# Kernel tuning notes

Hardware: AMD Instinct MI355X
Metric: run time of the kernel (lower is better)

## Reference

```python
import jax, jax.numpy as jnp
import numpy as np

D = 1024      # neural_dim
M = 8192      # memory_size (assumed fully used)
H = 16        # num_heads
B = 64        # batch
HD = D // H   # head dim


def setup_inputs() -> dict:
    key = jax.random.key(0)
    ks = jax.random.split(key, 24)
    s = 0.02
    inp = {
        "neural_input": jax.random.normal(ks[0], (B, D), jnp.float32),
        "memory_keys": jax.random.normal(ks[1], (M, D), jnp.float32),
        "memory_values": jax.random.normal(ks[2], (M, D), jnp.float32),
        # query/key/value projections (nn.Linear weights are [out, in])
        "Wq": jax.random.normal(ks[3], (D, D), jnp.float32) * s,
        "bq": jnp.zeros((D,), jnp.float32),
        "Wk": jax.random.normal(ks[4], (D, D), jnp.float32) * s,
        "bk": jnp.zeros((D,), jnp.float32),
        "Wv": jax.random.normal(ks[5], (D, D), jnp.float32) * s,
        "bv": jnp.zeros((D,), jnp.float32),
        # MultiheadAttention packed in-projection [3D, D] and out projection
        "in_proj_w": jax.random.normal(ks[6], (3 * D, D), jnp.float32) * s,
        "in_proj_b": jnp.zeros((3 * D,), jnp.float32),
        "out_w": jax.random.normal(ks[7], (D, D), jnp.float32) * s,
        "out_b": jnp.zeros((D,), jnp.float32),
        # memory_gate: Linear(2D->D), ReLU, Linear(D->D), Sigmoid
        "gW1": jax.random.normal(ks[8], (D, 2 * D), jnp.float32) * s,
        "gb1": jnp.zeros((D,), jnp.float32),
        "gW2": jax.random.normal(ks[9], (D, D), jnp.float32) * s,
        "gb2": jnp.zeros((D,), jnp.float32),
        # integration: Linear(2D->2D), ReLU, Linear(2D->D)
        "iW1": jax.random.normal(ks[10], (2 * D, 2 * D), jnp.float32) * s,
        "ib1": jnp.zeros((2 * D,), jnp.float32),
        "iW2": jax.random.normal(ks[11], (D, 2 * D), jnp.float32) * s,
        "ib2": jnp.zeros((D,), jnp.float32),
    }
    return inp


def reference(neural_input, memory_keys, memory_values,
              Wq, bq, Wk, bk, Wv, bv,
              in_proj_w, in_proj_b, out_w, out_b,
              gW1, gb1, gW2, gb2, iW1, ib1, iW2, ib2):
    x = neural_input  # [B, D]
    # pre-projections (memory_used assumed all True -> full tables)
    q = x @ Wq.T + bq                  # [B, D]
    k = memory_keys @ Wk.T + bk        # [M, D]
    v = memory_values @ Wv.T + bv      # [M, D]

    # MultiheadAttention (single query per batch element; K/V shared
    # across batch instead of the redundant expand in the original)
    Wiq, Wik, Wiv = in_proj_w[:D], in_proj_w[D:2 * D], in_proj_w[2 * D:]
    biq, bik, biv = in_proj_b[:D], in_proj_b[D:2 * D], in_proj_b[2 * D:]
    qh = (q @ Wiq.T + biq).reshape(B, H, HD)   # [B, H, hd]
    kh = (k @ Wik.T + bik).reshape(M, H, HD)   # [M, H, hd]
    vh = (v @ Wiv.T + biv).reshape(M, H, HD)   # [M, H, hd]

    scale = 1.0 / np.sqrt(HD).astype(np.float32)
    scores = jnp.einsum('bhd,mhd->bhm', qh, kh) * scale  # [B, H, M]
    attn = jax.nn.softmax(scores, axis=-1)
    ctx = jnp.einsum('bhm,mhd->bhd', attn, vh).reshape(B, D)
    memory_signal = ctx @ out_w.T + out_b      # [B, D]

    # gated fusion
    gate_in = jnp.concatenate([x, memory_signal], axis=-1)          # [B, 2D]
    gate = jax.nn.sigmoid(jax.nn.relu(gate_in @ gW1.T + gb1) @ gW2.T + gb2)
    gated_memory = gate * memory_signal
    combined = jnp.concatenate([x, gated_memory], axis=-1)          # [B, 2D]
    out = jax.nn.relu(combined @ iW1.T + ib1) @ iW2.T + ib2         # [B, D]
    return out
```

## Files before the change

kernel.cpp:

```cpp
#include <hip/hip_runtime.h>
#include <hip/hip_bf16.h>
#include <stdint.h>


typedef __bf16 bf16;
typedef __bf16 bf16x4 __attribute__((ext_vector_type(4)));
typedef __bf16 bf16x8 __attribute__((ext_vector_type(8)));
typedef float f32x4 __attribute__((ext_vector_type(4)));

#define D_ 1024
#define M_ 8192
#define B_ 64
#define H_ 16

static __device__ __forceinline__ void gload16(const void* g, void* l) {
  __builtin_amdgcn_global_load_lds(
      (const __attribute__((address_space(1))) void*)g,
      (__attribute__((address_space(3))) void*)l, 16, 0, 0);
}

static __device__ __forceinline__ f32x4 mfma16(bf16x8 a, bf16x8 b, f32x4 c) {
  return __builtin_amdgcn_mfma_f32_16x16x32_bf16(a, b, c, 0, 0, 0);
}

template <int U, int KLEN, typename OutT>
__device__ __forceinline__ void thin_gemm(
    const bf16* __restrict__ A, int lda,
    const bf16* __restrict__ Bm, int ldb,
    OutT* __restrict__ C, int ldc,
    const float* __restrict__ bias, float scale) {
  const int tid = threadIdx.x, lane = tid & 63, w = tid >> 6;
  const int rl = lane & 15, qq = lane >> 4;
  const bf16* pa = A + (int64_t)(w * 16 + rl) * lda + qq * 8;
  const bf16* pb[4];
  pb[0] = Bm + (int64_t)rl * ldb + qq * 8;
  pb[1] = pb[0] + (int64_t)16 * ldb;
  pb[2] = pb[0] + (int64_t)32 * ldb;
  pb[3] = pb[0] + (int64_t)48 * ldb;
  f32x4 acc[4] = {};
  bf16x8 av[2][U], bv[2][U][4];
#pragma unroll
  for (int u = 0; u < U; u++) {
    av[0][u] = *(const bf16x8*)(pa + u * 32);
#pragma unroll
    for (int j = 0; j < 4; j++)
      bv[0][u][j] = *(const bf16x8*)(pb[j] + u * 32);
  }
  constexpr int NI = KLEN / (32 * U);
#pragma unroll
  for (int it = 0; it < NI; it++) {
    const int cur = it & 1, nxt = cur ^ 1;
    if (it + 1 < NI) {
      int k = (it + 1) * 32 * U;
#pragma unroll
      for (int u = 0; u < U; u++) {
        av[nxt][u] = *(const bf16x8*)(pa + k + u * 32);
#pragma unroll
        for (int j = 0; j < 4; j++)
          bv[nxt][u][j] = *(const bf16x8*)(pb[j] + k + u * 32);
      }
    }
#pragma unroll
    for (int u = 0; u < U; u++)
#pragma unroll
      for (int j = 0; j < 4; j++)
        acc[j] = mfma16(av[cur][u], bv[cur][u][j], acc[j]);
  }
#pragma unroll
  for (int j = 0; j < 4; j++) {
    int gn = j * 16 + rl;
    float bb = bias ? bias[gn] : 0.0f;
#pragma unroll
    for (int r = 0; r < 4; r++) {
      int gm = w * 16 + qq * 4 + r;
      C[(int64_t)gm * ldc + gn] = (OutT)((acc[j][r] + bb) * scale);
    }
  }
}

struct CvtD { const float* src; bf16* dst; int end; };
struct PrepArgs {
  CvtD d[9];
  const float *Wq, *Wk, *Wv, *inw, *inb, *bq, *bk, *bv;
  const float *outb, *gb1, *gb2, *ib1, *ib2;
  bf16* WT;
  float *bc, *msR, *g1R, *gateR, *h1R, *out, *Oraw, *lmat;
};

__global__ __launch_bounds__(256) void prep_kernel(PrepArgs a) {
  const int bx = blockIdx.x, tid = threadIdx.x;
  if (bx < 29760) {
    int g = bx * 256 + tid;
    CvtD dd = a.d[8];
    int begin = a.d[7].end;
#pragma unroll
    for (int t = 7; t >= 0; t--)
      if (g < a.d[t].end) { dd = a.d[t]; begin = t ? a.d[t - 1].end : 0; }
    int i = (g - begin) * 4;
    float4 v = *(const float4*)(dd.src + i);
    bf16x4 o = { (bf16)v.x, (bf16)v.y, (bf16)v.z, (bf16)v.w };
    *(bf16x4*)(dd.dst + i) = o;
  } else if (bx < 32832) {
    int t = bx - 29760;
    int z = t >> 10, rem = t & 1023;
    const float* src = z == 0 ? a.Wq : z == 1 ? a.Wk : a.Wv;
    bf16* out = a.WT + (int64_t)z * D_ * D_;
    __shared__ bf16 tile[32][33];
    int tx = tid & 31, ty = tid >> 5;
    int r0 = (rem >> 5) * 32, c0 = (rem & 31) * 32;
#pragma unroll
    for (int i = 0; i < 32; i += 8)
      tile[ty + i][tx] = (bf16)src[(int64_t)(r0 + ty + i) * D_ + c0 + tx];
    __syncthreads();
#pragma unroll
    for (int i = 0; i < 32; i += 8)
      out[(int64_t)(c0 + ty + i) * D_ + r0 + tx] = tile[tx][ty + i];
  } else if (bx < 33600) {
    int t = bx - 32832;
    int w = tid >> 6, lane = tid & 63;
    int ng = t * 4 + w;
    int z = ng >> 10;
    const float* Wi = a.inw + (int64_t)ng * D_;
    const float* b = z == 0 ? a.bq : z == 1 ? a.bk : a.bv;
    float acc = 0.f;
#pragma unroll
    for (int l = 0; l < D_; l += 64) acc += Wi[l + lane] * b[l + lane];
#pragma unroll
    for (int m = 32; m; m >>= 1) acc += __shfl_xor(acc, m, 64);
    if (lane == 0) a.bc[ng] = acc + a.inb[ng];
  } else if (bx < 33984) {
    int t = bx - 33600;
    int seg = t >> 6, row = t & 63;
    int n = tid * 4;
    const float* b;
    float* dst;
    int bn = n;
    if (seg == 0)      { dst = a.msR   + row * 1024;        b = a.outb; }
    else if (seg == 1) { dst = a.g1R   + row * 1024;        b = a.gb1;  }
    else if (seg == 2) { dst = a.gateR + row * 1024;        b = a.gb2;  }
    else if (seg == 3) { dst = a.h1R   + row * 2048;        b = a.ib1;  }
    else if (seg == 4) { dst = a.h1R   + row * 2048 + 1024; b = a.ib1; bn = 1024 + n; }
    else               { dst = a.out   + row * 1024;        b = a.ib2;  }
    *(float4*)(dst + n) = *(const float4*)(b + bn);
  } else {
    int b = bx - 33984;
    float4 z4 = {0.f, 0.f, 0.f, 0.f};
    *(float4*)(a.Oraw + b * 1024 + tid * 4) = z4;
    if (b < 16 && tid < 64) a.lmat[b * 64 + tid] = 0.f;
  }
}

template <int MODE>
__global__ __launch_bounds__(256) void gemm_big(
    const bf16* __restrict__ A, int lda, int64_t sA,
    const bf16* __restrict__ Bm, int ldb, int64_t sB,
    bf16* __restrict__ C, int ldc, int64_t sC, bf16* __restrict__ Ct,
    const float* __restrict__ bias, int64_t sbias, int K,
    const bf16* __restrict__ qA, const bf16* __restrict__ qB,
    bf16* __restrict__ qC, const float* __restrict__ qbias) {
  int m0, n0, z;
  if (MODE == 0) {
    z = blockIdx.z; m0 = blockIdx.y * 128; n0 = blockIdx.x * 128;
  } else {
    if ((int)blockIdx.x >= 1024) {
      int n0q = ((int)blockIdx.x - 1024) * 64;
      thin_gemm<2, 1024, bf16>(qA, D_, qB + (int64_t)n0q * D_, D_,
                               qC + n0q, D_, qbias + n0q, 0.125f);
      return;
    }
    int lin = blockIdx.x, xcd = lin & 7, slot = lin >> 3;
    z = slot >> 6;
    int r = slot & 63;
    m0 = (xcd * 8 + (r >> 3)) * 128;
    n0 = (r & 7) * 128;
  }
  A += (int64_t)z * sA; Bm += (int64_t)z * sB;
  if (bias) bias += (int64_t)z * sbias;
  __shared__ alignas(16) bf16 As[128 * 32];
  __shared__ alignas(16) bf16 Bs[128 * 32];
  const int tid = threadIdx.x, lane = tid & 63, w = tid >> 6;
  const int wm = (w & 1) * 64, wn = (w >> 1) * 64;
  const int rl = lane & 15, qq = lane >> 4;
  f32x4 acc[4][4] = {};

  int c0 = w * 64 + lane, c1 = (4 + w) * 64 + lane;
  int ra0 = c0 >> 2, qa0 = (c0 & 3) ^ ((ra0 >> 1) & 3);
  int ra1 = c1 >> 2, qa1 = (c1 & 3) ^ ((ra1 >> 1) & 3);
  const bf16* gA0 = A + (int64_t)(m0 + ra0) * lda + qa0 * 8;
  const bf16* gA1 = A + (int64_t)(m0 + ra1) * lda + qa1 * 8;
  const bf16* gB0 = Bm + (int64_t)(n0 + ra0) * ldb + qa0 * 8;
  const bf16* gB1 = Bm + (int64_t)(n0 + ra1) * ldb + qa1 * 8;
  bf16* lA0 = As + w * 512;
  bf16* lA1 = As + (4 + w) * 512;
  bf16* lB0 = Bs + w * 512;
  bf16* lB1 = Bs + (4 + w) * 512;

  for (int k0 = 0; k0 < K; k0 += 32) {
    __syncthreads();
    gload16(gA0 + k0, lA0);
    gload16(gA1 + k0, lA1);
    gload16(gB0 + k0, lB0);
    gload16(gB1 + k0, lB1);
    __syncthreads();
    bf16x8 af[4], bb[4];
#pragma unroll
    for (int i = 0; i < 4; i++) {
      int r = wm + i * 16 + rl;
      af[i] = *(const bf16x8*)(As + r * 32 + (qq ^ ((r >> 1) & 3)) * 8);
    }
#pragma unroll
    for (int j = 0; j < 4; j++) {
      int r = wn + j * 16 + rl;
      bb[j] = *(const bf16x8*)(Bs + r * 32 + (qq ^ ((r >> 1) & 3)) * 8);
    }
#pragma unroll
    for (int i = 0; i < 4; i++)
#pragma unroll
      for (int j = 0; j < 4; j++)
        acc[i][j] = mfma16(af[i], bb[j], acc[i][j]);
  }
  if (MODE == 1 && z == 1) {
#pragma unroll
    for (int j = 0; j < 4; j++) {
      int gn = n0 + wn + j * 16 + rl;
      float bb2 = bias ? bias[gn] : 0.0f;
#pragma unroll
      for (int i = 0; i < 4; i++) {
        int gm0 = m0 + wm + i * 16 + qq * 4;
        f32x4 a = acc[i][j];
        bf16x4 o = { (bf16)(a[0] + bb2), (bf16)(a[1] + bb2),
                     (bf16)(a[2] + bb2), (bf16)(a[3] + bb2) };
        *(bf16x4*)(Ct + (int64_t)gn * M_ + gm0) = o;
      }
    }
  } else {
    C += (int64_t)z * sC;
#pragma unroll
    for (int j = 0; j < 4; j++) {
      int gn = n0 + wn + j * 16 + rl;
      float bb2 = bias ? bias[gn] : 0.0f;
#pragma unroll
      for (int i = 0; i < 4; i++) {
        int gm0 = m0 + wm + i * 16 + qq * 4;
#pragma unroll
        for (int r = 0; r < 4; r++)
          C[(int64_t)(gm0 + r) * ldc + gn] = (bf16)(acc[i][j][r] + bb2);
      }
    }
  }
}

__global__ __launch_bounds__(256, 2) void flash_kernel(
    const bf16* __restrict__ qh, const bf16* __restrict__ kh,
    const bf16* __restrict__ vhT, float* __restrict__ Oraw,
    float* __restrict__ lmat) {
  const int tid = threadIdx.x, lane = tid & 63, w = tid >> 6;
  const int rl = lane & 15, qq = lane >> 4;
  const int h = blockIdx.x >> 4, c = blockIdx.x & 15;
  __shared__ alignas(16) bf16 Plds[4 * 16 * 72];
  const bf16* qhp = qh + (int64_t)(w * 16 + rl) * D_ + h * 64 + qq * 8;
  bf16x8 aq0 = *(const bf16x8*)(qhp);
  bf16x8 aq1 = *(const bf16x8*)(qhp + 32);
  float lsum[4] = {0.f, 0.f, 0.f, 0.f};
  f32x4 acc_o[4] = {};
  bf16* pl = Plds + w * 1152;
  const bf16* khb = kh + (int64_t)(c * 512) * D_ + h * 64 + qq * 8;
  const bf16* vtb = vhT + (int64_t)(h * 64) * M_ + c * 512 + qq * 8;
  for (int nt = 0; nt < 8; nt++) {
    int mb = nt * 64;
    bf16x8 bk0[4], bk1[4], vv0[4], vv1[4];
#pragma unroll
    for (int j = 0; j < 4; j++) {
      const bf16* p = khb + (int64_t)(mb + j * 16 + rl) * D_;
      bk0[j] = *(const bf16x8*)(p);
      bk1[j] = *(const bf16x8*)(p + 32);
      const bf16* q = vtb + (int64_t)(j * 16 + rl) * M_ + mb;
      vv0[j] = *(const bf16x8*)(q);
      vv1[j] = *(const bf16x8*)(q + 32);
    }
    f32x4 s[4] = {};
#pragma unroll
    for (int j = 0; j < 4; j++) {
      s[j] = mfma16(aq0, bk0[j], s[j]);
      s[j] = mfma16(aq1, bk1[j], s[j]);
    }
#pragma unroll
    for (int j = 0; j < 4; j++)
#pragma unroll
      for (int r = 0; r < 4; r++) {
        float p = __expf(s[j][r]);
        lsum[r] += p;
        pl[(qq * 4 + r) * 72 + j * 16 + rl] = (bf16)p;
      }
    bf16x8 pa0 = *(const bf16x8*)(pl + rl * 72 + qq * 8);
    bf16x8 pa1 = *(const bf16x8*)(pl + rl * 72 + 32 + qq * 8);
#pragma unroll
    for (int j = 0; j < 4; j++) {
      acc_o[j] = mfma16(pa0, vv0[j], acc_o[j]);
      acc_o[j] = mfma16(pa1, vv1[j], acc_o[j]);
    }
  }
#pragma unroll
  for (int msk = 1; msk <= 8; msk <<= 1)
#pragma unroll
    for (int r = 0; r < 4; r++) lsum[r] += __shfl_xor(lsum[r], msk, 64);
#pragma unroll
  for (int j = 0; j < 4; j++)
#pragma unroll
    for (int r = 0; r < 4; r++)
      atomicAdd(&Oraw[(int64_t)(w * 16 + qq * 4 + r) * D_ + h * 64 + j * 16 + rl],
                acc_o[j][r]);
  if (rl == 0)
#pragma unroll
    for (int r = 0; r < 4; r++)
      atomicAdd(&lmat[h * 64 + w * 16 + qq * 4 + r], lsum[r]);
}

struct Chunk { const void* p0; const void* p1; int ld; int kind; };
struct StageArgs { Chunk c[16]; };

template <int NKK>
__global__ __launch_bounds__(256) void tail_stage(
    StageArgs sa, const bf16* __restrict__ Bw, int ldb,
    float* __restrict__ Craw, int ldc) {
  const int n0 = blockIdx.x * 64, kc = blockIdx.y;
  const int bk0 = kc * NKK * 32;
  const Chunk ch = sa.c[kc];
  const int tid = threadIdx.x, lane = tid & 63, w = tid >> 6;
  const int rl = lane & 15, qq = lane >> 4;
  const int m = w * 16 + rl;
  const bf16* pb[4];
#pragma unroll
  for (int j = 0; j < 4; j++)
    pb[j] = Bw + (int64_t)(n0 + j * 16 + rl) * ldb + bk0 + qq * 8;
  f32x4 acc[4] = {};
#pragma unroll
  for (int kk = 0; kk < NKK; kk++) {
    bf16x8 af;
    if (ch.kind == 0) {
      af = *(const bf16x8*)((const bf16*)ch.p0 + (int64_t)m * ch.ld +
                            kk * 32 + qq * 8);
    } else {
      const float* p = (const float*)ch.p0 + (int64_t)m * ch.ld + kk * 32 + qq * 8;
      float4 u0 = *(const float4*)p;
      float4 u1 = *(const float4*)(p + 4);
      if (ch.kind == 2) {
        u0.x = fmaxf(u0.x, 0.f); u0.y = fmaxf(u0.y, 0.f);
        u0.z = fmaxf(u0.z, 0.f); u0.w = fmaxf(u0.w, 0.f);
        u1.x = fmaxf(u1.x, 0.f); u1.y = fmaxf(u1.y, 0.f);
        u1.z = fmaxf(u1.z, 0.f); u1.w = fmaxf(u1.w, 0.f);
      } else if (ch.kind == 3) {
        const float* pm = (const float*)ch.p1 + (int64_t)m * ch.ld + kk * 32 + qq * 8;
        float4 m0 = *(const float4*)pm;
        float4 m1 = *(const float4*)(pm + 4);
        u0.x = m0.x / (1.f + __expf(-u0.x)); u0.y = m0.y / (1.f + __expf(-u0.y));
        u0.z = m0.z / (1.f + __expf(-u0.z)); u0.w = m0.w / (1.f + __expf(-u0.w));
        u1.x = m1.x / (1.f + __expf(-u1.x)); u1.y = m1.y / (1.f + __expf(-u1.y));
        u1.z = m1.z / (1.f + __expf(-u1.z)); u1.w = m1.w / (1.f + __expf(-u1.w));
      } else if (ch.kind == 4) {
        int hidx = (bk0 + kk * 32) >> 6;
        float linv = 1.0f / ((const float*)ch.p1)[hidx * 64 + m];
        u0.x *= linv; u0.y *= linv; u0.z *= linv; u0.w *= linv;
        u1.x *= linv; u1.y *= linv; u1.z *= linv; u1.w *= linv;
      }
      af = (bf16x8){ (bf16)u0.x, (bf16)u0.y, (bf16)u0.z, (bf16)u0.w,
                     (bf16)u1.x, (bf16)u1.y, (bf16)u1.z, (bf16)u1.w };
    }
    bf16x8 bf_[4];
#pragma unroll
    for (int j = 0; j < 4; j++) bf_[j] = *(const bf16x8*)(pb[j] + kk * 32);
#pragma unroll
    for (int j = 0; j < 4; j++) acc[j] = mfma16(af, bf_[j], acc[j]);
  }
#pragma unroll
  for (int j = 0; j < 4; j++) {
    int gn = n0 + j * 16 + rl;
#pragma unroll
    for (int r = 0; r < 4; r++) {
      int gm = w * 16 + qq * 4 + r;
      atomicAdd(&Craw[(int64_t)gm * ldc + gn], acc[j][r]);
    }
  }
}

extern "C" void kernel_launch(void* const* d_in, const int* in_sizes, int n_in,
                              void* d_out, int out_size, void* d_ws,
                              size_t ws_size, hipStream_t stream) {
  (void)in_sizes; (void)n_in; (void)out_size;
  const float* x    = (const float*)d_in[0];
  const float* mk   = (const float*)d_in[1];
  const float* mv   = (const float*)d_in[2];
  const float* Wq   = (const float*)d_in[3];
  const float* bq   = (const float*)d_in[4];
  const float* Wk   = (const float*)d_in[5];
  const float* bk   = (const float*)d_in[6];
  const float* Wv   = (const float*)d_in[7];
  const float* bv   = (const float*)d_in[8];
  const float* inw  = (const float*)d_in[9];
  const float* inb  = (const float*)d_in[10];
  const float* outw = (const float*)d_in[11];
  const float* outb = (const float*)d_in[12];
  const float* gW1  = (const float*)d_in[13];
  const float* gb1  = (const float*)d_in[14];
  const float* gW2  = (const float*)d_in[15];
  const float* gb2  = (const float*)d_in[16];
  const float* iW1  = (const float*)d_in[17];
  const float* ib1  = (const float*)d_in[18];
  const float* iW2  = (const float*)d_in[19];
  const float* ib2  = (const float*)d_in[20];

  char* ws = (char*)d_ws;
  size_t off = 0;
  auto alloc = [&](size_t bytes) {
    char* p = ws + off;
    off += (bytes + 255) & ~(size_t)255;
    return p;
  };
  bf16* mkmv  = (bf16*)alloc((size_t)2 * M_ * D_ * 2);
  bf16* inpj  = (bf16*)alloc((size_t)3 * D_ * D_ * 2);
  bf16* WT    = (bf16*)alloc((size_t)3 * D_ * D_ * 2);
  bf16* Wc    = (bf16*)alloc((size_t)3 * D_ * D_ * 2);
  float* bc   = (float*)alloc(3 * D_ * 4);
  bf16* xbf   = (bf16*)alloc((size_t)B_ * D_ * 2);
  bf16* qh    = (bf16*)alloc((size_t)B_ * D_ * 2);
  bf16* kh    = (bf16*)alloc((size_t)M_ * D_ * 2);
  bf16* vhT   = (bf16*)alloc((size_t)M_ * D_ * 2);
  float* Oraw = (float*)alloc((size_t)B_ * D_ * 4);
  float* lmat = (float*)alloc((size_t)H_ * B_ * 4);
  float* msR  = (float*)alloc((size_t)B_ * D_ * 4);
  float* g1R  = (float*)alloc((size_t)B_ * D_ * 4);
  float* gateR= (float*)alloc((size_t)B_ * D_ * 4);
  float* h1R  = (float*)alloc((size_t)B_ * 2 * D_ * 4);
  bf16* gW1b  = (bf16*)alloc((size_t)D_ * 2 * D_ * 2);
  bf16* gW2b  = (bf16*)alloc((size_t)D_ * D_ * 2);
  bf16* iW1b  = (bf16*)alloc((size_t)2 * D_ * 2 * D_ * 2);
  bf16* iW2b  = (bf16*)alloc((size_t)D_ * 2 * D_ * 2);
  bf16* outwb = (bf16*)alloc((size_t)D_ * D_ * 2);
  if (ws_size < off) return;

  PrepArgs pa;
  pa.d[0] = { mk,   mkmv,           2097152 };
  pa.d[1] = { mv,   mkmv + M_ * D_, 4194304 };
  pa.d[2] = { inw,  inpj,           4980736 };
  pa.d[3] = { gW1,  gW1b,           5505024 };
  pa.d[4] = { gW2,  gW2b,           5767168 };
  pa.d[5] = { iW1,  iW1b,           6815744 };
  pa.d[6] = { iW2,  iW2b,           7340032 };
  pa.d[7] = { outw, outwb,          7602176 };
  pa.d[8] = { x,    xbf,            7618560 };
  pa.Wq = Wq; pa.Wk = Wk; pa.Wv = Wv; pa.inw = inw; pa.inb = inb;
  pa.bq = bq; pa.bk = bk; pa.bv = bv;
  pa.outb = outb; pa.gb1 = gb1; pa.gb2 = gb2; pa.ib1 = ib1; pa.ib2 = ib2;
  pa.WT = WT; pa.bc = bc; pa.msR = msR; pa.g1R = g1R; pa.gateR = gateR;
  pa.h1R = h1R; pa.out = (float*)d_out; pa.Oraw = Oraw; pa.lmat = lmat;
  prep_kernel<<<dim3(34048), 256, 0, stream>>>(pa);

  gemm_big<0><<<dim3(8, 8, 3), 256, 0, stream>>>(
      inpj, D_, (int64_t)D_ * D_, WT, D_, (int64_t)D_ * D_,
      Wc, D_, (int64_t)D_ * D_, nullptr, nullptr, 0, D_,
      nullptr, nullptr, nullptr, nullptr);

  gemm_big<1><<<dim3(1040), 256, 0, stream>>>(
      mkmv, D_, (int64_t)M_ * D_, Wc + (int64_t)D_ * D_, D_, (int64_t)D_ * D_,
      kh, D_, 0, vhT, bc + D_, D_, D_,
      xbf, Wc, qh, bc);

  flash_kernel<<<dim3(256), 256, 0, stream>>>(qh, kh, vhT, Oraw, lmat);

  StageArgs s1;
  for (int kc = 0; kc < 8; kc++) s1.c[kc] = { Oraw + kc * 128, lmat, D_, 4 };
  tail_stage<4><<<dim3(16, 8), 256, 0, stream>>>(s1, outwb, D_, msR, D_);

  StageArgs s2;
  for (int kc = 0; kc < 8; kc++)  s2.c[kc] = { xbf + kc * 128, nullptr, D_, 0 };
  for (int kc = 8; kc < 16; kc++) s2.c[kc] = { msR + (kc - 8) * 128, nullptr, D_, 1 };
  tail_stage<4><<<dim3(16, 16), 256, 0, stream>>>(s2, gW1b, 2 * D_, g1R, D_);

  StageArgs s3;
  for (int kc = 0; kc < 8; kc++) s3.c[kc] = { g1R + kc * 128, nullptr, D_, 2 };
  tail_stage<4><<<dim3(16, 8), 256, 0, stream>>>(s3, gW2b, D_, gateR, D_);

  StageArgs s4;
  for (int kc = 0; kc < 8; kc++)  s4.c[kc] = { xbf + kc * 128, nullptr, D_, 0 };
  for (int kc = 8; kc < 16; kc++)
    s4.c[kc] = { gateR + (kc - 8) * 128, msR + (kc - 8) * 128, D_, 3 };
  tail_stage<4><<<dim3(32, 16), 256, 0, stream>>>(s4, iW1b, 2 * D_, h1R, 2 * D_);

  StageArgs s5;
  for (int kc = 0; kc < 16; kc++) s5.c[kc] = { h1R + kc * 128, nullptr, 2 * D_, 2 };
  tail_stage<4><<<dim3(16, 16), 256, 0, stream>>>(s5, iW2b, 2 * D_,
                                                  (float*)d_out, D_);
}
```

Baseline: 354.2 us.

## Replace big K/V projection GEMM with 256x256-tile 4-stage pipelined kernel

Adds a new gemm256 kernel that computes the memory-key and memory-value projections with 256x256 output tiles, 512 threads, and a 4-deep LDS ring buffer fed by direct global-to-LDS loads with XOR swizzle. Blocks are mapped so that tiles are grouped per XCD, and the q projection rides along in the first 16 blocks. Larger tiles raise arithmetic intensity and cut redundant operand traffic compared to the previous 1040-block launch, at the cost of 128KB dynamic LDS per block and a large register-resident accumulator, which limits occupancy to one block per CU. The v output is written transposed with 4-wide vector stores, while the k output still uses scalar stores.

```diff
diff --git a/kernel.cpp b/kernel.cpp
--- a/kernel.cpp
+++ b/kernel.cpp
@@ -248,6 +248,146 @@
       }
     }
   }
+}
+
+__global__ __launch_bounds__(512) void gemm256(
+    const bf16* __restrict__ A,
+    const bf16* __restrict__ Wc,
+    const float* __restrict__ bc,
+    bf16* __restrict__ kh, bf16* __restrict__ vhT,
+    const bf16* __restrict__ qA, const bf16* __restrict__ qB,
+    bf16* __restrict__ qC, const float* __restrict__ qbias) {
+  extern __shared__ __align__(16) bf16 lds[];
+  const int bid = blockIdx.x;
+  if (bid < 16) {
+    if (threadIdx.x < 256) {
+      int n0q = bid * 64;
+      thin_gemm<2, 1024, bf16>(qA, D_, qB + (int64_t)n0q * D_, D_,
+                               qC + n0q, D_, qbias + n0q, 0.125f);
+    }
+    return;
+  }
+  const int lin = bid - 16;
+  const int xcd = lin & 7, s = lin >> 3;
+  const int z = xcd >> 2;
+  const int m0 = ((xcd & 3) * 8 + (s >> 2)) * 256;
+  const int n0 = (s & 3) * 256;
+  const bf16* Ab = A + (int64_t)z * M_ * D_;
+  const bf16* Bb = Wc + (int64_t)(z + 1) * D_ * D_;
+  const float* bias = bc + (z + 1) * D_;
+
+  const int tid = threadIdx.x, lane = tid & 63, w = tid >> 6;
+  const int rl = lane & 15, qq = lane >> 4;
+  const int wr = w >> 2, wcn = w & 3;
+
+  const int ci0 = w * 128 + lane, ci1 = ci0 + 64;
+  const int ra0 = ci0 >> 2, ca0 = (ci0 & 3) ^ ((ra0 >> 1) & 3);
+  const int ra1 = ci1 >> 2, ca1 = (ci1 & 3) ^ ((ra1 >> 1) & 3);
+  const bf16* gA0 = Ab + (int64_t)(m0 + ra0) * D_ + ca0 * 8;
+  const bf16* gA1 = Ab + (int64_t)(m0 + ra1) * D_ + ca1 * 8;
+  const bf16* gB0 = Bb + (int64_t)(n0 + ra0) * D_ + ca0 * 8;
+  const bf16* gB1 = Bb + (int64_t)(n0 + ra1) * D_ + ca1 * 8;
+  const int lA0 = w * 1024, lA1 = lA0 + 512;
+
+#define STAGE3(kt)                                   \
+  do {                                               \
+    bf16* bse = lds + ((kt) & 3) * 16384;            \
+    int ko = (kt) * 32;                              \
+    gload16(gA0 + ko, bse + lA0);                    \
+    gload16(gA1 + ko, bse + lA1);                    \
+    gload16(gB0 + ko, bse + 8192 + lA0);             \
+    gload16(gB1 + ko, bse + 8192 + lA1);             \
+  } while (0)
+#define FENCE3 asm volatile("" ::: "memory")
+#define BARRIER3                       \
+  do {                                 \
+    FENCE3;                            \
+    __builtin_amdgcn_s_barrier();      \
+    FENCE3;                            \
+  } while (0)
+
+  f32x4 acc[8][4] = {};
+  const int sq8 = (qq ^ ((rl >> 1) & 3)) * 8;
+
+  auto compute = [&](int kt) {
+    const bf16* ba = lds + (kt & 3) * 16384;
+    const bf16* bbp = ba + 8192;
+    bf16x8 bfr[4], afr[4];
+#pragma unroll
+    for (int j = 0; j < 4; j++)
+      bfr[j] = *(const bf16x8*)(bbp + (wcn * 64 + j * 16 + rl) * 32 + sq8);
+#pragma unroll
+    for (int mi = 0; mi < 4; mi++)
+      afr[mi] = *(const bf16x8*)(ba + (wr * 128 + mi * 16 + rl) * 32 + sq8);
+    __builtin_amdgcn_s_setprio(1);
+#pragma unroll
+    for (int mi = 0; mi < 4; mi++)
+#pragma unroll
+      for (int j = 0; j < 4; j++)
+        acc[mi][j] = mfma16(afr[mi], bfr[j], acc[mi][j]);
+    __builtin_amdgcn_s_setprio(0);
+#pragma unroll
+    for (int mi = 0; mi < 4; mi++)
+      afr[mi] = *(const bf16x8*)(ba + (wr * 128 + (mi + 4) * 16 + rl) * 32 + sq8);
+    __builtin_amdgcn_s_setprio(1);
+#pragma unroll
+    for (int mi = 0; mi < 4; mi++)
+#pragma unroll
+      for (int j = 0; j < 4; j++)
+        acc[mi + 4][j] = mfma16(afr[mi], bfr[j], acc[mi + 4][j]);
+    __builtin_amdgcn_s_setprio(0);
+  };
+
+  constexpr int NT = 32;
+  STAGE3(0);
+  STAGE3(1);
+  STAGE3(2);
+#pragma unroll 1
+  for (int kt = 0; kt < NT - 2; kt++) {
+    if (kt + 3 < NT) STAGE3(kt + 3);
+    asm volatile("s_waitcnt vmcnt(8)" ::: "memory");
+    BARRIER3;
+    compute(kt);
+    BARRIER3;
+  }
+  asm volatile("s_waitcnt vmcnt(4)" ::: "memory");
+  BARRIER3;
+  compute(NT - 2);
+  asm volatile("s_waitcnt vmcnt(0)" ::: "memory");
+  BARRIER3;
+  compute(NT - 1);
+
+  if (z == 0) {
+#pragma unroll
+    for (int j = 0; j < 4; j++) {
+      int gn = n0 + wcn * 64 + j * 16 + rl;
+      float bb2 = bias[gn];
+#pragma unroll
+      for (int mi = 0; mi < 8; mi++) {
+        int gm0 = m0 + wr * 128 + mi * 16 + qq * 4;
+#pragma unroll
+        for (int r = 0; r < 4; r++)
+          kh[(int64_t)(gm0 + r) * D_ + gn] = (bf16)(acc[mi][j][r] + bb2);
+      }
+    }
+  } else {
+#pragma unroll
+    for (int j = 0; j < 4; j++) {
+      int gn = n0 + wcn * 64 + j * 16 + rl;
+      float bb2 = bias[gn];
+#pragma unroll
+      for (int mi = 0; mi < 8; mi++) {
+        int gm0 = m0 + wr * 128 + mi * 16 + qq * 4;
+        f32x4 a = acc[mi][j];
+        bf16x4 o = { (bf16)(a[0] + bb2), (bf16)(a[1] + bb2),
+                     (bf16)(a[2] + bb2), (bf16)(a[3] + bb2) };
+        *(bf16x4*)(vhT + (int64_t)gn * M_ + gm0) = o;
+      }
+    }
+  }
+#undef STAGE3
+#undef FENCE3
+#undef BARRIER3
 }
 
 __global__ __launch_bounds__(256, 2) void flash_kernel(
@@ -460,10 +600,10 @@
       Wc, D_, (int64_t)D_ * D_, nullptr, nullptr, 0, D_,
       nullptr, nullptr, nullptr, nullptr);
 
-  gemm_big<1><<<dim3(1040), 256, 0, stream>>>(
-      mkmv, D_, (int64_t)M_ * D_, Wc + (int64_t)D_ * D_, D_, (int64_t)D_ * D_,
-      kh, D_, 0, vhT, bc + D_, D_, D_,
-      xbf, Wc, qh, bc);
+  hipFuncSetAttribute((const void*)gemm256,
+                      hipFuncAttributeMaxDynamicSharedMemorySize, 131072);
+  gemm256<<<dim3(272), dim3(512), 131072, stream>>>(
+      mkmv, Wc, bc, kh, vhT, xbf, Wc, qh, bc);
 
   flash_kernel<<<dim3(256), 256, 0, stream>>>(qh, kh, vhT, Oraw, lmat);
 
```

Measured after the change: 343.7 us. -3.0%, faster.

## Add triple-buffered 128x256 K/V projection GEMM and widen prep conversion per thread

Applied to the files above, without the earlier changes.

The K/V projection GEMM moves into a dedicated kernel with 128x256 tiles and three LDS stages filled by async global-to-LDS loads. It waits on explicit vmcnt counts and raises MFMA priority, so loads overlap compute and fewer blocks re-read the weights. The tile-to-XCD mapping is also reworked. The prep kernel now converts 32 floats per thread instead of 4, which cuts the fp32-to-bf16 conversion launch from about 30k blocks to about 3.7k. The cost is 72KB of dynamic LDS per block and lower occupancy, plus a hard-coded K loop count tied to D=1024.

```diff
diff --git a/kernel.cpp b/kernel.cpp
--- a/kernel.cpp
+++ b/kernel.cpp
@@ -89,19 +89,25 @@
 
 __global__ __launch_bounds__(256) void prep_kernel(PrepArgs a) {
   const int bx = blockIdx.x, tid = threadIdx.x;
-  if (bx < 29760) {
-    int g = bx * 256 + tid;
+  if (bx < 3720) {
     CvtD dd = a.d[8];
     int begin = a.d[7].end;
 #pragma unroll
     for (int t = 7; t >= 0; t--)
-      if (g < a.d[t].end) { dd = a.d[t]; begin = t ? a.d[t - 1].end : 0; }
-    int i = (g - begin) * 4;
-    float4 v = *(const float4*)(dd.src + i);
-    bf16x4 o = { (bf16)v.x, (bf16)v.y, (bf16)v.z, (bf16)v.w };
-    *(bf16x4*)(dd.dst + i) = o;
-  } else if (bx < 32832) {
-    int t = bx - 29760;
+      if (bx < a.d[t].end) { dd = a.d[t]; begin = t ? a.d[t - 1].end : 0; }
+    int64_t i = (int64_t)(bx - begin) * 8192 + tid * 32;
+    const float* src = dd.src + i;
+    bf16* dst = dd.dst + i;
+    float4 v[8];
+#pragma unroll
+    for (int u = 0; u < 8; u++) v[u] = *(const float4*)(src + u * 4);
+#pragma unroll
+    for (int u = 0; u < 8; u++) {
+      bf16x4 o = { (bf16)v[u].x, (bf16)v[u].y, (bf16)v[u].z, (bf16)v[u].w };
+      *(bf16x4*)(dst + u * 4) = o;
+    }
+  } else if (bx < 6792) {
+    int t = bx - 3720;
     int z = t >> 10, rem = t & 1023;
     const float* src = z == 0 ? a.Wq : z == 1 ? a.Wk : a.Wv;
     bf16* out = a.WT + (int64_t)z * D_ * D_;
@@ -115,8 +121,8 @@
 #pragma unroll
     for (int i = 0; i < 32; i += 8)
       out[(int64_t)(c0 + ty + i) * D_ + r0 + tx] = tile[tx][ty + i];
-  } else if (bx < 33600) {
-    int t = bx - 32832;
+  } else if (bx < 7560) {
+    int t = bx - 6792;
     int w = tid >> 6, lane = tid & 63;
     int ng = t * 4 + w;
     int z = ng >> 10;
@@ -128,8 +134,8 @@
 #pragma unroll
     for (int m = 32; m; m >>= 1) acc += __shfl_xor(acc, m, 64);
     if (lane == 0) a.bc[ng] = acc + a.inb[ng];
-  } else if (bx < 33984) {
-    int t = bx - 33600;
+  } else if (bx < 7944) {
+    int t = bx - 7560;
     int seg = t >> 6, row = t & 63;
     int n = tid * 4;
     const float* b;
@@ -143,39 +149,19 @@
     else               { dst = a.out   + row * 1024;        b = a.ib2;  }
     *(float4*)(dst + n) = *(const float4*)(b + bn);
   } else {
-    int b = bx - 33984;
+    int b = bx - 7944;
     float4 z4 = {0.f, 0.f, 0.f, 0.f};
     *(float4*)(a.Oraw + b * 1024 + tid * 4) = z4;
     if (b < 16 && tid < 64) a.lmat[b * 64 + tid] = 0.f;
   }
 }
 
-template <int MODE>
 __global__ __launch_bounds__(256) void gemm_big(
     const bf16* __restrict__ A, int lda, int64_t sA,
     const bf16* __restrict__ Bm, int ldb, int64_t sB,
-    bf16* __restrict__ C, int ldc, int64_t sC, bf16* __restrict__ Ct,
-    const float* __restrict__ bias, int64_t sbias, int K,
-    const bf16* __restrict__ qA, const bf16* __restrict__ qB,
-    bf16* __restrict__ qC, const float* __restrict__ qbias) {
-  int m0, n0, z;
-  if (MODE == 0) {
-    z = blockIdx.z; m0 = blockIdx.y * 128; n0 = blockIdx.x * 128;
-  } else {
-    if ((int)blockIdx.x >= 1024) {
-      int n0q = ((int)blockIdx.x - 1024) * 64;
-      thin_gemm<2, 1024, bf16>(qA, D_, qB + (int64_t)n0q * D_, D_,
-                               qC + n0q, D_, qbias + n0q, 0.125f);
-      return;
-    }
-    int lin = blockIdx.x, xcd = lin & 7, slot = lin >> 3;
-    z = slot >> 6;
-    int r = slot & 63;
-    m0 = (xcd * 8 + (r >> 3)) * 128;
-    n0 = (r & 7) * 128;
-  }
+    bf16* __restrict__ C, int ldc, int64_t sC, int K) {
+  const int z = blockIdx.z, m0 = blockIdx.y * 128, n0 = blockIdx.x * 128;
   A += (int64_t)z * sA; Bm += (int64_t)z * sB;
-  if (bias) bias += (int64_t)z * sbias;
   __shared__ alignas(16) bf16 As[128 * 32];
   __shared__ alignas(16) bf16 Bs[128 * 32];
   const int tid = threadIdx.x, lane = tid & 63, w = tid >> 6;
@@ -219,32 +205,142 @@
       for (int j = 0; j < 4; j++)
         acc[i][j] = mfma16(af[i], bb[j], acc[i][j]);
   }
-  if (MODE == 1 && z == 1) {
+  C += (int64_t)z * sC;
+#pragma unroll
+  for (int j = 0; j < 4; j++) {
+    int gn = n0 + wn + j * 16 + rl;
+#pragma unroll
+    for (int i = 0; i < 4; i++) {
+      int gm0 = m0 + wm + i * 16 + qq * 4;
+#pragma unroll
+      for (int r = 0; r < 4; r++)
+        C[(int64_t)(gm0 + r) * ldc + gn] = (bf16)acc[i][j][r];
+    }
+  }
+}
+
+__global__ __launch_bounds__(256) void gemm_kv(
+    const bf16* __restrict__ A,
+    const bf16* __restrict__ Wc,
+    const float* __restrict__ bc,
+    bf16* __restrict__ kh, bf16* __restrict__ vhT,
+    const bf16* __restrict__ qA, const bf16* __restrict__ qB,
+    bf16* __restrict__ qC, const float* __restrict__ qbias) {
+  extern __shared__ __align__(16) bf16 lds[];
+  const int bid = blockIdx.x;
+  if (bid >= 512) {
+    int n0q = (bid - 512) * 64;
+    thin_gemm<2, 1024, bf16>(qA, D_, qB + (int64_t)n0q * D_, D_,
+                             qC + n0q, D_, qbias + n0q, 0.125f);
+    return;
+  }
+  const int xcd = bid & 7, s = bid >> 3;
+  const int z = xcd >> 2;
+  const int m0 = ((xcd & 3) * 16 + (s >> 2)) * 128;
+  const int n0 = (s & 3) * 256;
+  const bf16* Ab = A + (int64_t)z * M_ * D_;
+  const bf16* Bb = Wc + (int64_t)(z + 1) * D_ * D_;
+  const float* bias = bc + (z + 1) * D_;
+
+  const int tid = threadIdx.x, lane = tid & 63, w = tid >> 6;
+  const int rl = lane & 15, qq = lane >> 4;
+
+  const bf16* gA0_; const bf16* gA1_;
+  const bf16* gB_[4];
+  {
+    int ci0 = w * 64 + lane, ci1 = ci0 + 256;
+    int r0 = ci0 >> 2, c0 = (ci0 & 3) ^ ((r0 >> 1) & 3);
+    int r1 = ci1 >> 2, c1 = (ci1 & 3) ^ ((r1 >> 1) & 3);
+    gA0_ = Ab + (int64_t)(m0 + r0) * D_ + c0 * 8;
+    gA1_ = Ab + (int64_t)(m0 + r1) * D_ + c1 * 8;
+#pragma unroll
+    for (int s2 = 0; s2 < 4; s2++) {
+      int ci = w * 64 + lane + s2 * 256;
+      int rb = ci >> 2, cb = (ci & 3) ^ ((rb >> 1) & 3);
+      gB_[s2] = Bb + (int64_t)(n0 + rb) * D_ + cb * 8;
+    }
+  }
+  const int lA0 = w * 512, lA1 = w * 512 + 2048;
+  const int lB0 = 4096 + w * 512;
+
+  f32x4 acc[8][4] = {};
+  bf16x8 bfr[4], afr[8];
+  const int sq8 = (qq ^ ((rl >> 1) & 3)) * 8;
+
+#define SCB __builtin_amdgcn_sched_barrier(0)
+#define BARR __builtin_amdgcn_s_barrier()
+#define VMW(N) asm volatile("s_waitcnt vmcnt(" #N ")")
+
+#define STG(BUF, KT)                                  \
+  do {                                                \
+    bf16* b_ = lds + (BUF) * 12288;                   \
+    int ko_ = (KT) * 32;                              \
+    gload16(gA0_ + ko_, b_ + lA0);                    \
+    gload16(gA1_ + ko_, b_ + lA1);                    \
+    gload16(gB_[0] + ko_, b_ + lB0);                  \
+    gload16(gB_[1] + ko_, b_ + lB0 + 2048);           \
+    gload16(gB_[2] + ko_, b_ + lB0 + 4096);           \
+    gload16(gB_[3] + ko_, b_ + lB0 + 6144);           \
+  } while (0)
+
+#define COMP(BUF)                                                            \
+  do {                                                                       \
+    const bf16* ba_ = lds + (BUF) * 12288;                                   \
+    const bf16* bb_ = ba_ + 4096;                                            \
+    for (int j = 0; j < 4; j++)                                              \
+      bfr[j] = *(const bf16x8*)(bb_ + (w * 64 + j * 16 + rl) * 32 + sq8);    \
+    for (int mi = 0; mi < 8; mi++)                                           \
+      afr[mi] = *(const bf16x8*)(ba_ + (mi * 16 + rl) * 32 + sq8);           \
+    __builtin_amdgcn_s_setprio(1);                                           \
+    for (int mi = 0; mi < 8; mi++)                                           \
+      for (int j = 0; j < 4; j++)                                            \
+        acc[mi][j] = mfma16(afr[mi], bfr[j], acc[mi][j]);                    \
+    __builtin_amdgcn_s_setprio(0);                                           \
+  } while (0)
+
+  STG(0, 0);
+  STG(1, 1);
+#pragma unroll 1
+  for (int t = 0; t < 10; t++) {
+    const int kb = t * 3;
+    VMW(6); SCB; BARR; SCB; STG(2, kb + 2); COMP(0);
+    VMW(6); SCB; BARR; SCB; STG(0, kb + 3); COMP(1);
+    VMW(6); SCB; BARR; SCB; STG(1, kb + 4); COMP(2);
+  }
+  VMW(6); SCB; BARR; SCB; COMP(0);
+  VMW(0); SCB; BARR; SCB; COMP(1);
+
+#undef SCB
+#undef BARR
+#undef VMW
+#undef STG
+#undef COMP
+
+  if (z == 0) {
 #pragma unroll
     for (int j = 0; j < 4; j++) {
-      int gn = n0 + wn + j * 16 + rl;
-      float bb2 = bias ? bias[gn] : 0.0f;
-#pragma unroll
-      for (int i = 0; i < 4; i++) {
-        int gm0 = m0 + wm + i * 16 + qq * 4;
-        f32x4 a = acc[i][j];
+      int gn = n0 + w * 64 + j * 16 + rl;
+      float bb2 = bias[gn];
+#pragma unroll
+      for (int mi = 0; mi < 8; mi++) {
+        int gm0 = m0 + mi * 16 + qq * 4;
+#pragma unroll
+        for (int r = 0; r < 4; r++)
+          kh[(int64_t)(gm0 + r) * D_ + gn] = (bf16)(acc[mi][j][r] + bb2);
+      }
+    }
+  } else {
+#pragma unroll
+    for (int j = 0; j < 4; j++) {
+      int gn = n0 + w * 64 + j * 16 + rl;
+      float bb2 = bias[gn];
+#pragma unroll
+      for (int mi = 0; mi < 8; mi++) {
+        int gm0 = m0 + mi * 16 + qq * 4;
+        f32x4 a = acc[mi][j];
         bf16x4 o = { (bf16)(a[0] + bb2), (bf16)(a[1] + bb2),
                      (bf16)(a[2] + bb2), (bf16)(a[3] + bb2) };
-        *(bf16x4*)(Ct + (int64_t)gn * M_ + gm0) = o;
-      }
-    }
-  } else {
-    C += (int64_t)z * sC;
-#pragma unroll
-    for (int j = 0; j < 4; j++) {
-      int gn = n0 + wn + j * 16 + rl;
-      float bb2 = bias ? bias[gn] : 0.0f;
-#pragma unroll
-      for (int i = 0; i < 4; i++) {
-        int gm0 = m0 + wm + i * 16 + qq * 4;
-#pragma unroll
-        for (int r = 0; r < 4; r++)
-          C[(int64_t)(gm0 + r) * ldc + gn] = (bf16)(acc[i][j][r] + bb2);
+        *(bf16x4*)(vhT + (int64_t)gn * M_ + gm0) = o;
       }
     }
   }
@@ -439,31 +535,30 @@
   if (ws_size < off) return;
 
   PrepArgs pa;
-  pa.d[0] = { mk,   mkmv,           2097152 };
-  pa.d[1] = { mv,   mkmv + M_ * D_, 4194304 };
-  pa.d[2] = { inw,  inpj,           4980736 };
-  pa.d[3] = { gW1,  gW1b,           5505024 };
-  pa.d[4] = { gW2,  gW2b,           5767168 };
-  pa.d[5] = { iW1,  iW1b,           6815744 };
-  pa.d[6] = { iW2,  iW2b,           7340032 };
-  pa.d[7] = { outw, outwb,          7602176 };
-  pa.d[8] = { x,    xbf,            7618560 };
+  pa.d[0] = { mk,   mkmv,           1024 };
+  pa.d[1] = { mv,   mkmv + M_ * D_, 2048 };
+  pa.d[2] = { inw,  inpj,           2432 };
+  pa.d[3] = { gW1,  gW1b,           2688 };
+  pa.d[4] = { gW2,  gW2b,           2816 };
+  pa.d[5] = { iW1,  iW1b,           3328 };
+  pa.d[6] = { iW2,  iW2b,           3584 };
+  pa.d[7] = { outw, outwb,          3712 };
+  pa.d[8] = { x,    xbf,            3720 };
   pa.Wq = Wq; pa.Wk = Wk; pa.Wv = Wv; pa.inw = inw; pa.inb = inb;
   pa.bq = bq; pa.bk = bk; pa.bv = bv;
   pa.outb = outb; pa.gb1 = gb1; pa.gb2 = gb2; pa.ib1 = ib1; pa.ib2 = ib2;
   pa.WT = WT; pa.bc = bc; pa.msR = msR; pa.g1R = g1R; pa.gateR = gateR;
   pa.h1R = h1R; pa.out = (float*)d_out; pa.Oraw = Oraw; pa.lmat = lmat;
-  prep_kernel<<<dim3(34048), 256, 0, stream>>>(pa);
-
-  gemm_big<0><<<dim3(8, 8, 3), 256, 0, stream>>>(
+  prep_kernel<<<dim3(8008), 256, 0, stream>>>(pa);
+
+  gemm_big<<<dim3(8, 8, 3), 256, 0, stream>>>(
       inpj, D_, (int64_t)D_ * D_, WT, D_, (int64_t)D_ * D_,
-      Wc, D_, (int64_t)D_ * D_, nullptr, nullptr, 0, D_,
-      nullptr, nullptr, nullptr, nullptr);
-
-  gemm_big<1><<<dim3(1040), 256, 0, stream>>>(
-      mkmv, D_, (int64_t)M_ * D_, Wc + (int64_t)D_ * D_, D_, (int64_t)D_ * D_,
-      kh, D_, 0, vhT, bc + D_, D_, D_,
-      xbf, Wc, qh, bc);
+      Wc, D_, (int64_t)D_ * D_, D_);
+
+  hipFuncSetAttribute((const void*)gemm_kv,
+                      hipFuncAttributeMaxDynamicSharedMemorySize, 73728);
+  gemm_kv<<<dim3(528), dim3(256), 73728, stream>>>(
+      mkmv, Wc, bc, kh, vhT, xbf, Wc, qh, bc);
 
   flash_kernel<<<dim3(256), 256, 0, stream>>>(qh, kh, vhT, Oraw, lmat);
 
```

Result: no change. 351.0 us (-0.9%).
